# Optimization experiments

Hardware: AMD Instinct MI355X
Metric: run time of the kernel (lower is better)

Reference implementation:

```python
import jax, jax.numpy as jnp
import numpy as np

EPS = 1e-12


def agnn_layer(x, row, col, num_nodes):
    """AGNN propagation with beta frozen at 1.0 (requires_grad=False in source).
    alpha_ij = softmax_{j in N(i)} ( beta * cos(x_i, x_j) ); out_i = sum_j alpha_ij * x_j.
    row = destination node of each edge (segment id), col = source node.
    """
    xn = x / (jnp.linalg.norm(x, axis=-1, keepdims=True) + EPS)  # unit-norm features
    score = jnp.sum(xn[row] * xn[col], axis=-1)                   # [E] beta=1 * cos sim
    smax = jax.ops.segment_max(score, row, num_segments=num_nodes)
    e = jnp.exp(score - smax[row])                                # stable softmax numerator
    denom = jax.ops.segment_sum(e, row, num_segments=num_nodes)
    alpha = e / jnp.maximum(denom[row], EPS)                      # [E]
    out = jax.ops.segment_sum(alpha[:, None] * x[col], row, num_segments=num_nodes)
    return out


def setup_inputs() -> dict:
    key = jax.random.key(0)
    ks = jax.random.split(key, 8)
    N, E = 100000, 1600000
    IN_DIM, HID, OUT_DIM = 128, 64, 64
    x = jax.random.normal(ks[0], (N, IN_DIM), dtype=jnp.float32)
    edge_row = jnp.sort(jax.random.randint(ks[1], (E,), 0, N))
    edge_col = jax.random.randint(ks[2], (E,), 0, N)
    # Linear params (PyTorch nn.Linear style: y = x @ W.T + b)
    s1 = 1.0 / np.sqrt(IN_DIM)
    W1 = jax.random.uniform(ks[3], (HID, IN_DIM), jnp.float32, -s1, s1)
    b1 = jax.random.uniform(ks[4], (HID,), jnp.float32, -s1, s1)
    s2 = 1.0 / np.sqrt(HID)
    W2 = jax.random.uniform(ks[5], (OUT_DIM, HID), jnp.float32, -s2, s2)
    b2 = jax.random.uniform(ks[6], (OUT_DIM,), jnp.float32, -s2, s2)
    return {"x": x, "edge_row": edge_row, "edge_col": edge_col,
            "W1": W1, "b1": b1, "W2": W2, "b2": b2}


def reference(x, edge_row, edge_col, W1, b1, W2, b2):
    N = x.shape[0]
    h = jax.nn.relu(x @ W1.T + b1)
    for _ in range(4):  # 4 frozen-beta AGNN layers
        h = jax.nn.relu(agnn_layer(h, edge_row, edge_col, N))
    return h @ W2.T + b2
```

## Files before the change

kernel.cpp:

```cpp
#include <hip/hip_runtime.h>


typedef _Float16 h2 __attribute__((ext_vector_type(2)));

union U4H { uint4 u; h2 h[4]; };
union U2H { uint2 u; h2 h[2]; };
union UHI { unsigned u; h2 h; };

#define DEV_INLINE __device__ __forceinline__

DEV_INLINE h2 mkh2(float a, float b) {
    h2 r; r.x = (_Float16)a; r.y = (_Float16)b; return r;
}

__global__ __launch_bounds__(256) void build_rowptr(const int* __restrict__ row,
                                                    int* __restrict__ ptr,
                                                    int N, int E) {
    int i = blockIdx.x * blockDim.x + threadIdx.x;
    if (i > N) return;
    int lo = 0, hi = E;
    while (lo < hi) {
        int mid = (lo + hi) >> 1;
        if (row[mid] < i) lo = mid + 1; else hi = mid;
    }
    ptr[i] = lo;
}

__global__ __launch_bounds__(256) void gemm1_relu(const float* __restrict__ x,
                                                  const float* __restrict__ W1,
                                                  const float* __restrict__ b1,
                                                  unsigned short* __restrict__ xn,
                                                  float* __restrict__ nrm,
                                                  int N) {
    __shared__ __align__(16) float Wt[64 * 64];
    __shared__ __align__(16) float xT[64 * 64];
    const int tid  = threadIdx.x;
    const int tx   = tid & 15;
    const int ty   = tid >> 4;
    const int base = blockIdx.x * 64;

    float4 b4 = ((const float4*)b1)[tx];
    float4 acc[4];
    acc[0] = b4; acc[1] = b4; acc[2] = b4; acc[3] = b4;

    for (int kc = 0; kc < 128; kc += 64) {
        if (kc) __syncthreads();
        const float4* W4 = (const float4*)W1;
        for (int idx = tid; idx < 64 * 16; idx += 256) {
            int o = idx & 63, k4 = idx >> 6;
            float4 v = W4[o * 32 + (kc >> 2) + k4];
            Wt[(4 * k4 + 0) * 64 + o] = v.x;
            Wt[(4 * k4 + 1) * 64 + o] = v.y;
            Wt[(4 * k4 + 2) * 64 + o] = v.z;
            Wt[(4 * k4 + 3) * 64 + o] = v.w;
        }
        const float4* x4p = (const float4*)x;
        for (int idx = tid; idx < 64 * 16; idx += 256) {
            int mm = idx & 63, k4 = idx >> 6;
            int node = base + mm;
            float4 v = make_float4(0.f, 0.f, 0.f, 0.f);
            if (node < N) v = x4p[(size_t)node * 32 + (kc >> 2) + k4];
            xT[(4 * k4 + 0) * 64 + mm] = v.x;
            xT[(4 * k4 + 1) * 64 + mm] = v.y;
            xT[(4 * k4 + 2) * 64 + mm] = v.z;
            xT[(4 * k4 + 3) * 64 + mm] = v.w;
        }
        __syncthreads();

#pragma unroll 4
        for (int k = 0; k < 64; ++k) {
            const float4 w4 = *(const float4*)&Wt[k * 64 + 4 * tx];
            const float4 xv = *(const float4*)&xT[k * 64 + 4 * ty];
            acc[0].x = fmaf(xv.x, w4.x, acc[0].x);
            acc[0].y = fmaf(xv.x, w4.y, acc[0].y);
            acc[0].z = fmaf(xv.x, w4.z, acc[0].z);
            acc[0].w = fmaf(xv.x, w4.w, acc[0].w);
            acc[1].x = fmaf(xv.y, w4.x, acc[1].x);
            acc[1].y = fmaf(xv.y, w4.y, acc[1].y);
            acc[1].z = fmaf(xv.y, w4.z, acc[1].z);
            acc[1].w = fmaf(xv.y, w4.w, acc[1].w);
            acc[2].x = fmaf(xv.z, w4.x, acc[2].x);
            acc[2].y = fmaf(xv.z, w4.y, acc[2].y);
            acc[2].z = fmaf(xv.z, w4.z, acc[2].z);
            acc[2].w = fmaf(xv.z, w4.w, acc[2].w);
            acc[3].x = fmaf(xv.w, w4.x, acc[3].x);
            acc[3].y = fmaf(xv.w, w4.y, acc[3].y);
            acc[3].z = fmaf(xv.w, w4.z, acc[3].z);
            acc[3].w = fmaf(xv.w, w4.w, acc[3].w);
        }
    }

#pragma unroll
    for (int mm = 0; mm < 4; ++mm) {
        float4 r = acc[mm];
        r.x = fmaxf(r.x, 0.f); r.y = fmaxf(r.y, 0.f);
        r.z = fmaxf(r.z, 0.f); r.w = fmaxf(r.w, 0.f);
        float s = fmaf(r.x, r.x, fmaf(r.y, r.y, fmaf(r.z, r.z, r.w * r.w)));
        s += __shfl_xor(s, 1, 64);
        s += __shfl_xor(s, 2, 64);
        s += __shfl_xor(s, 4, 64);
        s += __shfl_xor(s, 8, 64);
        const float nn  = sqrtf(s) + 1e-12f;
        const float inv = 1.f / nn;
        int node = base + 4 * ty + mm;
        if (node < N) {
            U2H pk;
            pk.h[0] = mkh2(r.x * inv, r.y * inv);
            pk.h[1] = mkh2(r.z * inv, r.w * inv);
            *(uint2*)&xn[(size_t)node * 64 + 4 * tx] = pk.u;
            if (tx == mm) nrm[node] = nn;
        }
    }
}

__global__ __launch_bounds__(256) void agnn_layer(const uint4* __restrict__ xn4,
                                                  const float* __restrict__ nrm,
                                                  const int* __restrict__ ptr,
                                                  const int* __restrict__ col,
                                                  uint4* __restrict__ xo4,
                                                  float* __restrict__ nrmo,
                                                  int N) {
    const int tid  = threadIdx.x;
    const int lane = tid & 63;
    const int g    = (lane >> 3) & 3;
    const int sub  = lane & 7;
    const int i    = blockIdx.x * 8 + (tid >> 5);
    if (i >= N) return;

    U4H hi_;
    hi_.u = xn4[(unsigned)i * 8u + sub];
    {
        const _Float16 L2E = (_Float16)1.4426950408889634f;
        h2 l2 = {L2E, L2E};
#pragma unroll
        for (int t = 0; t < 4; ++t) hi_.h[t] *= l2;
    }

    const int p0 = ptr[i], p1 = ptr[i + 1];

    float den = 0.f;
    U4H acc;
    acc.h[0] = mkh2(0.f, 0.f); acc.h[1] = mkh2(0.f, 0.f);
    acc.h[2] = mkh2(0.f, 0.f); acc.h[3] = mkh2(0.f, 0.f);

#define EDGE_BODY(VU, NRMJ)                                                  \
    {                                                                        \
        U4H xa; xa.u = (VU);                                                 \
        float s = 0.f;                                                       \
        s = __builtin_amdgcn_fdot2(hi_.h[0], xa.h[0], s, false);             \
        s = __builtin_amdgcn_fdot2(hi_.h[1], xa.h[1], s, false);             \
        s = __builtin_amdgcn_fdot2(hi_.h[2], xa.h[2], s, false);             \
        s = __builtin_amdgcn_fdot2(hi_.h[3], xa.h[3], s, false);             \
        s += __shfl_xor(s, 1, 64);                                           \
        s += __shfl_xor(s, 2, 64);                                           \
        s += __shfl_xor(s, 4, 64);                                           \
        const float p = exp2f(s);                                            \
        den += p;                                                            \
        const _Float16 wh = (_Float16)(p * (NRMJ));                          \
        h2 w2 = {wh, wh};                                                    \
        acc.h[0] += w2 * xa.h[0];                                            \
        acc.h[1] += w2 * xa.h[1];                                            \
        acc.h[2] += w2 * xa.h[2];                                            \
        acc.h[3] += w2 * xa.h[3];                                            \
    }

    int e = p0 + g;
    for (; e + 4 < p1; e += 8) {
        const int ja = col[e];
        const int jb = col[e + 4];
        const uint4 va = xn4[(unsigned)ja * 8u + sub];
        const uint4 vb = xn4[(unsigned)jb * 8u + sub];
        const float na = nrm[ja];
        const float nb = nrm[jb];
        EDGE_BODY(va, na)
        EDGE_BODY(vb, nb)
    }
    if (e < p1) {
        const int j = col[e];
        const uint4 v = xn4[(unsigned)j * 8u + sub];
        const float nj = nrm[j];
        EDGE_BODY(v, nj)
    }
#undef EDGE_BODY

#pragma unroll
    for (int off = 8; off <= 16; off <<= 1) {
        den += __shfl_xor(den, off, 64);
#pragma unroll
        for (int t = 0; t < 4; ++t) {
            UHI a; a.h = acc.h[t];
            UHI b; b.u = (unsigned)__shfl_xor((int)a.u, off, 64);
            acc.h[t] = a.h + b.h;
        }
    }

    const float id = 1.f / fmaxf(den, 1e-12f);
    float o[8];
#pragma unroll
    for (int t = 0; t < 4; ++t) {
        o[2 * t]     = fmaxf((float)acc.h[t].x * id, 0.f);
        o[2 * t + 1] = fmaxf((float)acc.h[t].y * id, 0.f);
    }

    float s2 = 0.f;
#pragma unroll
    for (int t = 0; t < 8; ++t) s2 = fmaf(o[t], o[t], s2);
    s2 += __shfl_xor(s2, 1, 64);
    s2 += __shfl_xor(s2, 2, 64);
    s2 += __shfl_xor(s2, 4, 64);
    const float nn  = sqrtf(s2) + 1e-12f;
    const float inv = 1.f / nn;

    if (g == 0) {
        U4H ov;
        ov.h[0] = mkh2(o[0] * inv, o[1] * inv);
        ov.h[1] = mkh2(o[2] * inv, o[3] * inv);
        ov.h[2] = mkh2(o[4] * inv, o[5] * inv);
        ov.h[3] = mkh2(o[6] * inv, o[7] * inv);
        xo4[(unsigned)i * 8u + sub] = ov.u;
        if (sub == 0) nrmo[i] = nn;
    }
}

__global__ __launch_bounds__(256) void gemm2(const unsigned short* __restrict__ xn,
                                             const float* __restrict__ nrm,
                                             const float* __restrict__ W2,
                                             const float* __restrict__ b2,
                                             float* __restrict__ out,
                                             int N) {
    __shared__ __align__(16) float Wt[64 * 64];
    __shared__ __align__(16) float xT[64 * 64];
    const int tid  = threadIdx.x;
    const int tx   = tid & 15;
    const int ty   = tid >> 4;
    const int base = blockIdx.x * 64;

    {
        const float4* W4 = (const float4*)W2;
        for (int idx = tid; idx < 64 * 16; idx += 256) {
            int o = idx & 63, k4 = idx >> 6;
            float4 v = W4[o * 16 + k4];
            Wt[(4 * k4 + 0) * 64 + o] = v.x;
            Wt[(4 * k4 + 1) * 64 + o] = v.y;
            Wt[(4 * k4 + 2) * 64 + o] = v.z;
            Wt[(4 * k4 + 3) * 64 + o] = v.w;
        }
        const uint2* x2 = (const uint2*)xn;
        for (int idx = tid; idx < 64 * 16; idx += 256) {
            int mm = idx & 63, k4 = idx >> 6;
            int node = base + mm;
            U2H v; v.u = make_uint2(0u, 0u);
            float nn = 0.f;
            if (node < N) { v.u = x2[(size_t)node * 16 + k4]; nn = nrm[node]; }
            xT[(4 * k4 + 0) * 64 + mm] = (float)v.h[0].x * nn;
            xT[(4 * k4 + 1) * 64 + mm] = (float)v.h[0].y * nn;
            xT[(4 * k4 + 2) * 64 + mm] = (float)v.h[1].x * nn;
            xT[(4 * k4 + 3) * 64 + mm] = (float)v.h[1].y * nn;
        }
    }
    __syncthreads();

    float4 b4 = ((const float4*)b2)[tx];
    float4 acc[4];
    acc[0] = b4; acc[1] = b4; acc[2] = b4; acc[3] = b4;

#pragma unroll 4
    for (int k = 0; k < 64; ++k) {
        const float4 w4 = *(const float4*)&Wt[k * 64 + 4 * tx];
        const float4 xv = *(const float4*)&xT[k * 64 + 4 * ty];
        acc[0].x = fmaf(xv.x, w4.x, acc[0].x);
        acc[0].y = fmaf(xv.x, w4.y, acc[0].y);
        acc[0].z = fmaf(xv.x, w4.z, acc[0].z);
        acc[0].w = fmaf(xv.x, w4.w, acc[0].w);
        acc[1].x = fmaf(xv.y, w4.x, acc[1].x);
        acc[1].y = fmaf(xv.y, w4.y, acc[1].y);
        acc[1].z = fmaf(xv.y, w4.z, acc[1].z);
        acc[1].w = fmaf(xv.y, w4.w, acc[1].w);
        acc[2].x = fmaf(xv.z, w4.x, acc[2].x);
        acc[2].y = fmaf(xv.z, w4.y, acc[2].y);
        acc[2].z = fmaf(xv.z, w4.z, acc[2].z);
        acc[2].w = fmaf(xv.z, w4.w, acc[2].w);
        acc[3].x = fmaf(xv.w, w4.x, acc[3].x);
        acc[3].y = fmaf(xv.w, w4.y, acc[3].y);
        acc[3].z = fmaf(xv.w, w4.z, acc[3].z);
        acc[3].w = fmaf(xv.w, w4.w, acc[3].w);
    }

#pragma unroll
    for (int mm = 0; mm < 4; ++mm) {
        int node = base + 4 * ty + mm;
        if (node < N) *(float4*)&out[(size_t)node * 64 + 4 * tx] = acc[mm];
    }
}

extern "C" void kernel_launch(void* const* d_in, const int* in_sizes, int n_in,
                              void* d_out, int out_size, void* d_ws, size_t ws_size,
                              hipStream_t stream) {
    const float* x   = (const float*)d_in[0];
    const int*   row = (const int*)d_in[1];
    const int*   col = (const int*)d_in[2];
    const float* W1  = (const float*)d_in[3];
    const float* b1  = (const float*)d_in[4];
    const float* W2  = (const float*)d_in[5];
    const float* b2  = (const float*)d_in[6];
    float* out = (float*)d_out;

    const int N = in_sizes[0] / 128;
    const int E = in_sizes[1];

    char* ws = (char*)d_ws;
    size_t off = 0;
    unsigned short* ha = (unsigned short*)(ws + off); off += (size_t)N * 64 * 2;
    unsigned short* hb = (unsigned short*)(ws + off); off += (size_t)N * 64 * 2;
    float* na_ = (float*)(ws + off); off += (size_t)N * sizeof(float);
    float* nb_ = (float*)(ws + off); off += (size_t)N * sizeof(float);
    int*   ptr = (int*)  (ws + off); off += (size_t)(N + 1) * sizeof(int);
    (void)ws_size; (void)n_in; (void)out_size;

    build_rowptr<<<(N + 256) / 256, 256, 0, stream>>>(row, ptr, N, E);

    const int nbG = (N + 63) / 64;
    gemm1_relu<<<nbG, 256, 0, stream>>>(x, W1, b1, ha, na_, N);

    const int nb8 = (N + 7) / 8;
    unsigned short* hc = ha; unsigned short* hn = hb;
    float* nc = na_; float* nn = nb_;
    for (int l = 0; l < 4; ++l) {
        agnn_layer<<<nb8, 256, 0, stream>>>((const uint4*)hc, nc, ptr, col,
                                            (uint4*)hn, nn, N);
        unsigned short* t = hc; hc = hn; hn = t;
        float* tf = nc; nc = nn; nn = tf;
    }

    gemm2<<<nbG, 256, 0, stream>>>(hc, nc, W2, b2, out, N);
}
```

Measured before the change: 306.1 us.

## Sort nodes by degree and assign 16 lanes per node in AGNN layer

Adds a counting-sort pipeline (histogram, scan, scatter) that builds a permutation of nodes grouped by in-degree. The AGNN kernel then processes nodes in this order so wavefronts hold nodes of similar degree, which reduces divergence. It also cuts the lanes per node from 32 to 16 (2 edge groups instead of 4), packing more nodes into each block. Separately, the GEMM1 shared tiles shrink from a 64-wide to a 32-wide K chunk. The trade-offs are four extra small kernel launches and scattered node order, which lowers locality for output writes and the self-feature loads.

```diff
diff --git a/kernel.cpp b/kernel.cpp
--- a/kernel.cpp
+++ b/kernel.cpp
@@ -26,14 +26,55 @@
     ptr[i] = lo;
 }
 
+__global__ __launch_bounds__(1024) void hist_zero(int* __restrict__ hist) {
+    hist[threadIdx.x] = 0;
+}
+
+__global__ __launch_bounds__(256) void hist_build(const int* __restrict__ ptr,
+                                                  int* __restrict__ hist, int N) {
+    int i = blockIdx.x * blockDim.x + threadIdx.x;
+    if (i >= N) return;
+    int d = ptr[i + 1] - ptr[i];
+    if (d > 1023) d = 1023;
+    atomicAdd(&hist[d], 1);
+}
+
+__global__ __launch_bounds__(1024) void scan_hist(const int* __restrict__ hist,
+                                                  int* __restrict__ offs) {
+    __shared__ int a[1024], b[1024];
+    const int t = threadIdx.x;
+    const int h = hist[t];
+    a[t] = h;
+    __syncthreads();
+    int* src = a; int* dst = b;
+    for (int off = 1; off < 1024; off <<= 1) {
+        int v = src[t] + (t >= off ? src[t - off] : 0);
+        dst[t] = v;
+        __syncthreads();
+        int* tmp = src; src = dst; dst = tmp;
+    }
+    offs[t] = src[t] - h;
+}
+
+__global__ __launch_bounds__(256) void scatter_perm(const int* __restrict__ ptr,
+                                                    int* __restrict__ offs,
+                                                    int* __restrict__ perm, int N) {
+    int i = blockIdx.x * blockDim.x + threadIdx.x;
+    if (i >= N) return;
+    int d = ptr[i + 1] - ptr[i];
+    if (d > 1023) d = 1023;
+    int pos = atomicAdd(&offs[d], 1);
+    perm[pos] = i;
+}
+
 __global__ __launch_bounds__(256) void gemm1_relu(const float* __restrict__ x,
                                                   const float* __restrict__ W1,
                                                   const float* __restrict__ b1,
                                                   unsigned short* __restrict__ xn,
                                                   float* __restrict__ nrm,
                                                   int N) {
-    __shared__ __align__(16) float Wt[64 * 64];
-    __shared__ __align__(16) float xT[64 * 64];
+    __shared__ __align__(16) float Wt[32 * 64];
+    __shared__ __align__(16) float xT[32 * 64];
     const int tid  = threadIdx.x;
     const int tx   = tid & 15;
     const int ty   = tid >> 4;
@@ -43,10 +84,10 @@
     float4 acc[4];
     acc[0] = b4; acc[1] = b4; acc[2] = b4; acc[3] = b4;
 
-    for (int kc = 0; kc < 128; kc += 64) {
+    for (int kc = 0; kc < 128; kc += 32) {
         if (kc) __syncthreads();
         const float4* W4 = (const float4*)W1;
-        for (int idx = tid; idx < 64 * 16; idx += 256) {
+        for (int idx = tid; idx < 32 * 16; idx += 256) {
             int o = idx & 63, k4 = idx >> 6;
             float4 v = W4[o * 32 + (kc >> 2) + k4];
             Wt[(4 * k4 + 0) * 64 + o] = v.x;
@@ -55,7 +96,7 @@
             Wt[(4 * k4 + 3) * 64 + o] = v.w;
         }
         const float4* x4p = (const float4*)x;
-        for (int idx = tid; idx < 64 * 16; idx += 256) {
+        for (int idx = tid; idx < 32 * 16; idx += 256) {
             int mm = idx & 63, k4 = idx >> 6;
             int node = base + mm;
             float4 v = make_float4(0.f, 0.f, 0.f, 0.f);
@@ -68,7 +109,7 @@
         __syncthreads();
 
 #pragma unroll 4
-        for (int k = 0; k < 64; ++k) {
+        for (int k = 0; k < 32; ++k) {
             const float4 w4 = *(const float4*)&Wt[k * 64 + 4 * tx];
             const float4 xv = *(const float4*)&xT[k * 64 + 4 * ty];
             acc[0].x = fmaf(xv.x, w4.x, acc[0].x);
@@ -117,15 +158,17 @@
                                                   const float* __restrict__ nrm,
                                                   const int* __restrict__ ptr,
                                                   const int* __restrict__ col,
+                                                  const int* __restrict__ perm,
                                                   uint4* __restrict__ xo4,
                                                   float* __restrict__ nrmo,
                                                   int N) {
     const int tid  = threadIdx.x;
     const int lane = tid & 63;
-    const int g    = (lane >> 3) & 3;
+    const int g    = (lane >> 3) & 1;
     const int sub  = lane & 7;
-    const int i    = blockIdx.x * 8 + (tid >> 5);
-    if (i >= N) return;
+    const int slot = blockIdx.x * 16 + (tid >> 4);
+    if (slot >= N) return;
+    const int i = perm[slot];
 
     U4H hi_;
     hi_.u = xn4[(unsigned)i * 8u + sub];
@@ -165,9 +208,9 @@
     }
 
     int e = p0 + g;
-    for (; e + 4 < p1; e += 8) {
+    for (; e + 2 < p1; e += 4) {
         const int ja = col[e];
-        const int jb = col[e + 4];
+        const int jb = col[e + 2];
         const uint4 va = xn4[(unsigned)ja * 8u + sub];
         const uint4 vb = xn4[(unsigned)jb * 8u + sub];
         const float na = nrm[ja];
@@ -183,13 +226,12 @@
     }
 #undef EDGE_BODY
 
-#pragma unroll
-    for (int off = 8; off <= 16; off <<= 1) {
-        den += __shfl_xor(den, off, 64);
+    {
+        den += __shfl_xor(den, 8, 64);
 #pragma unroll
         for (int t = 0; t < 4; ++t) {
             UHI a; a.h = acc.h[t];
-            UHI b; b.u = (unsigned)__shfl_xor((int)a.u, off, 64);
+            UHI b; b.u = (unsigned)__shfl_xor((int)a.u, 8, 64);
             acc.h[t] = a.h + b.h;
         }
     }
@@ -312,22 +354,31 @@
     size_t off = 0;
     unsigned short* ha = (unsigned short*)(ws + off); off += (size_t)N * 64 * 2;
     unsigned short* hb = (unsigned short*)(ws + off); off += (size_t)N * 64 * 2;
-    float* na_ = (float*)(ws + off); off += (size_t)N * sizeof(float);
-    float* nb_ = (float*)(ws + off); off += (size_t)N * sizeof(float);
-    int*   ptr = (int*)  (ws + off); off += (size_t)(N + 1) * sizeof(int);
+    float* na_  = (float*)(ws + off); off += (size_t)N * sizeof(float);
+    float* nb_  = (float*)(ws + off); off += (size_t)N * sizeof(float);
+    int*   ptr  = (int*)  (ws + off); off += (size_t)(N + 1) * sizeof(int);
+    off = (off + 15) & ~(size_t)15;
+    int*   hist = (int*)  (ws + off); off += 1024 * sizeof(int);
+    int*   offs = (int*)  (ws + off); off += 1024 * sizeof(int);
+    int*   perm = (int*)  (ws + off); off += (size_t)N * sizeof(int);
     (void)ws_size; (void)n_in; (void)out_size;
 
     build_rowptr<<<(N + 256) / 256, 256, 0, stream>>>(row, ptr, N, E);
+
+    hist_zero<<<1, 1024, 0, stream>>>(hist);
+    hist_build<<<(N + 255) / 256, 256, 0, stream>>>(ptr, hist, N);
+    scan_hist<<<1, 1024, 0, stream>>>(hist, offs);
+    scatter_perm<<<(N + 255) / 256, 256, 0, stream>>>(ptr, offs, perm, N);
 
     const int nbG = (N + 63) / 64;
     gemm1_relu<<<nbG, 256, 0, stream>>>(x, W1, b1, ha, na_, N);
 
-    const int nb8 = (N + 7) / 8;
+    const int nb16 = (N + 15) / 16;
     unsigned short* hc = ha; unsigned short* hn = hb;
     float* nc = na_; float* nn = nb_;
     for (int l = 0; l < 4; ++l) {
-        agnn_layer<<<nb8, 256, 0, stream>>>((const uint4*)hc, nc, ptr, col,
-                                            (uint4*)hn, nn, N);
+        agnn_layer<<<nb16, 256, 0, stream>>>((const uint4*)hc, nc, ptr, col, perm,
+                                             (uint4*)hn, nn, N);
         unsigned short* t = hc; hc = hn; hn = t;
         float* tf = nc; nc = nn; nn = tf;
     }
```

Result: slower. 882.0 us (+188.1%).
